# Optimization experiments

Measured on AMD Instinct MI355X. Metric: run time of the kernel, lower is better.

Reference implementation:

```python
import jax, jax.numpy as jnp
import numpy as np


def setup_inputs() -> dict:
    key = jax.random.key(0)
    k1, k2 = jax.random.split(key)
    num_tokens, top_k, num_experts = 1048576, 8, 64
    top_scores = jax.random.uniform(k1, (num_tokens, top_k), dtype=jnp.float32)
    selected_experts_indices = jax.random.randint(
        k2, (num_tokens, top_k), 0, num_experts, dtype=jnp.int64
    ) if jax.config.jax_enable_x64 else jax.random.randint(
        k2, (num_tokens, top_k), 0, num_experts, dtype=jnp.int32
    )
    return {
        "top_scores": top_scores,
        "selected_experts_indices": selected_experts_indices,
        "num_experts": num_experts,
    }


def reference(top_scores, selected_experts_indices, num_experts):
    flat_idx = selected_experts_indices.reshape(-1)  # [num_tokens*top_k]
    # histogram of tokens per expert (torch.histc returns float)
    num_tokens_per_expert = jnp.bincount(flat_idx, length=num_experts).astype(jnp.float32)
    # stable argsort by expert id -> permutation grouping tokens by expert
    token_indices_experts_sorted = jnp.argsort(flat_idx, stable=True)
    # gather routing scores into expert-sorted order
    top_scores_experts_sorted = top_scores.reshape(-1)[token_indices_experts_sorted]
    return (
        top_scores_experts_sorted,
        token_indices_experts_sorted,
        num_tokens_per_expert,
    )
```

## Files before the change

kernel.cpp:

```cpp
#include <hip/hip_runtime.h>


#define TILE 4096
#define WAVES 8
#define WCH  512
#define RND  8
#define TPB  512

__device__ __forceinline__ unsigned long long match_mask(
    unsigned key,
    unsigned long long b0, unsigned long long b1, unsigned long long b2,
    unsigned long long b3, unsigned long long b4, unsigned long long b5,
    unsigned long long am) {
  unsigned long long m = am;
  m &= (key & 1u)  ? b0 : ~b0;
  m &= (key & 2u)  ? b1 : ~b1;
  m &= (key & 4u)  ? b2 : ~b2;
  m &= (key & 8u)  ? b3 : ~b3;
  m &= (key & 16u) ? b4 : ~b4;
  m &= (key & 32u) ? b5 : ~b5;
  return m;
}

__global__ __launch_bounds__(256) void hist_kernel(
    const int* __restrict__ idx, unsigned* __restrict__ countsT,
    int N, int nb) {
  __shared__ unsigned h[4][64];
  const int wave = threadIdx.x >> 6;
  const int lane = threadIdx.x & 63;

  long long base = (long long)blockIdx.x * TILE;
  long long rem = (long long)N - base;
  unsigned cnt = 0;

  if (rem >= TILE) {
    const int4* v = (const int4*)(idx + base);
    unsigned es[16];
    #pragma unroll
    for (int k = 0; k < 4; ++k) {
      int4 x = v[threadIdx.x + k * 256];
      es[k * 4 + 0] = ((unsigned)x.x) & 63u;
      es[k * 4 + 1] = ((unsigned)x.y) & 63u;
      es[k * 4 + 2] = ((unsigned)x.z) & 63u;
      es[k * 4 + 3] = ((unsigned)x.w) & 63u;
    }
    #pragma unroll
    for (int r = 0; r < 16; ++r) {
      unsigned e = es[r];
      unsigned long long b0 = __ballot(e & 1u);
      unsigned long long b1 = __ballot(e & 2u);
      unsigned long long b2 = __ballot(e & 4u);
      unsigned long long b3 = __ballot(e & 8u);
      unsigned long long b4 = __ballot(e & 16u);
      unsigned long long b5 = __ballot(e & 32u);
      cnt += (unsigned)__popcll(
          match_mask((unsigned)lane, b0, b1, b2, b3, b4, b5, ~0ull));
    }
  } else {
    long long wstart = base + (long long)wave * 1024;
    for (int r = 0; r < 16; ++r) {
      long long i = wstart + (long long)r * 64 + lane;
      bool valid = i < (long long)N;
      unsigned long long am = __ballot(valid ? 1 : 0);
      unsigned e = valid ? (((unsigned)idx[i]) & 63u) : 0u;
      unsigned long long b0 = __ballot(e & 1u);
      unsigned long long b1 = __ballot(e & 2u);
      unsigned long long b2 = __ballot(e & 4u);
      unsigned long long b3 = __ballot(e & 8u);
      unsigned long long b4 = __ballot(e & 16u);
      unsigned long long b5 = __ballot(e & 32u);
      cnt += (unsigned)__popcll(
          match_mask((unsigned)lane, b0, b1, b2, b3, b4, b5, am));
    }
  }

  h[wave][lane] = cnt;
  __syncthreads();
  if (threadIdx.x < 64) {
    countsT[(size_t)blockIdx.x * 64 + threadIdx.x] =
        h[0][threadIdx.x] + h[1][threadIdx.x] + h[2][threadIdx.x] + h[3][threadIdx.x];
  }
}

__global__ __launch_bounds__(256) void scan_kernel(
    unsigned* __restrict__ countsT, unsigned* __restrict__ totals,
    float* __restrict__ out_counts, int nb) {
  const int e = blockIdx.x;
  const int t = threadIdx.x;
  const int wave = t >> 6;
  const int lane = t & 63;

  __shared__ unsigned buf[2048];
  __shared__ unsigned wsum[4];

  unsigned carry = 0;
  for (int c = 0; c < nb; c += 2048) {
    int m = nb - c; if (m > 2048) m = 2048;
    for (int j = t; j < 2048; j += 256)
      buf[j] = (j < m) ? countsT[(size_t)(c + j) * 64 + e] : 0u;
    __syncthreads();
    unsigned v[8]; unsigned s = 0;
    #pragma unroll
    for (int k = 0; k < 8; ++k) { v[k] = buf[t * 8 + k]; s += v[k]; }
    unsigned inc = s;
    #pragma unroll
    for (int d = 1; d < 64; d <<= 1) {
      unsigned nv = __shfl_up(inc, d, 64);
      if (lane >= d) inc += nv;
    }
    if (lane == 63) wsum[wave] = inc;
    __syncthreads();
    unsigned woff = 0;
    for (int w = 0; w < wave; ++w) woff += wsum[w];
    unsigned btot = wsum[0] + wsum[1] + wsum[2] + wsum[3];
    unsigned run = carry + woff + (inc - s);
    #pragma unroll
    for (int k = 0; k < 8; ++k) { buf[t * 8 + k] = run; run += v[k]; }
    __syncthreads();
    for (int j = t; j < 2048; j += 256)
      if (j < m) countsT[(size_t)(c + j) * 64 + e] = buf[j];
    carry += btot;
    __syncthreads();
  }
  if (t == 0) {
    totals[e] = carry;
    out_counts[e] = (float)carry;
  }
}

__global__ __launch_bounds__(TPB, 8) void scatter_kernel(
    const int* __restrict__ idx, const float* __restrict__ scores,
    const unsigned* __restrict__ baseT, const unsigned* __restrict__ totals,
    float* __restrict__ out_scores, float* __restrict__ out_idx,
    int N, int nb) {
  __shared__ __align__(16) uint2 sdat[TILE];
  __shared__ __align__(16) unsigned char tmpb[WAVES][64][RND];
  __shared__ unsigned shc[WAVES][64];
  __shared__ unsigned gdest[64];

  const int t = threadIdx.x;
  const int wave = t >> 6;
  const int lane = t & 63;
  const unsigned long long lt = (1ull << lane) - 1ull;

  const long long base = (long long)blockIdx.x * TILE;
  const long long start = base + (long long)wave * WCH;
  const bool fullt = (base + TILE) <= (long long)N;

  const unsigned tot = totals[lane];
  const unsigned gb0 = baseT[(size_t)blockIdx.x * 64 + lane];

  unsigned e_pk[2] = {0, 0};
  unsigned r_pk[2] = {0, 0};
  float    sreg[RND];
  unsigned c_pk[2];
  unsigned wtotal = 0;

  unsigned* idxs = (unsigned*)sdat;

  if (fullt) {
    {
      const int4* gi = (const int4*)(idx + base);
      int4 a0 = gi[t];
      int4 a1 = gi[t + 512];
      #pragma unroll
      for (int r = 0; r < RND; ++r) sreg[r] = scores[start + r * 64 + lane];
      ((int4*)idxs)[t] = a0;
      ((int4*)idxs)[t + 512] = a1;
    }
    *(uint2*)(&tmpb[wave][lane][0]) = make_uint2(0u, 0u);
    __syncthreads();

    #pragma unroll
    for (int r = 0; r < RND; ++r) {
      unsigned e = idxs[wave * WCH + r * 64 + lane] & 63u;
      unsigned long long b0 = __ballot(e & 1u);
      unsigned long long b1 = __ballot(e & 2u);
      unsigned long long b2 = __ballot(e & 4u);
      unsigned long long b3 = __ballot(e & 8u);
      unsigned long long b4 = __ballot(e & 16u);
      unsigned long long b5 = __ballot(e & 32u);
      unsigned long long ms = match_mask(e, b0, b1, b2, b3, b4, b5, ~0ull);
      unsigned rank = (unsigned)__popcll(ms & lt);
      unsigned rcnt = (unsigned)__popcll(ms);
      if (rank == 0) tmpb[wave][e][r] = (unsigned char)rcnt;
      const int q = r >> 2, sh = (r & 3) * 8;
      e_pk[q] |= e << sh;
      r_pk[q] |= rank << sh;
    }
    uint2 cw = *(const uint2*)(&tmpb[wave][lane][0]);
    c_pk[0] = cw.x; c_pk[1] = cw.y;
  } else {
    for (int j = t; j < TILE; j += TPB) sdat[j].y = 0xFFFFFFFFu;
    *(uint2*)(&tmpb[wave][lane][0]) = make_uint2(0u, 0u);
    __syncthreads();
    for (int r = 0; r < RND; ++r) {
      long long i = start + (long long)r * 64 + lane;
      bool valid = i < (long long)N;
      unsigned long long am = __ballot(valid ? 1 : 0);
      unsigned e = valid ? (((unsigned)idx[i]) & 63u) : 0u;
      sreg[r] = valid ? scores[i] : 0.0f;
      unsigned long long b0 = __ballot(e & 1u);
      unsigned long long b1 = __ballot(e & 2u);
      unsigned long long b2 = __ballot(e & 4u);
      unsigned long long b3 = __ballot(e & 8u);
      unsigned long long b4 = __ballot(e & 16u);
      unsigned long long b5 = __ballot(e & 32u);
      unsigned long long ms = match_mask(e, b0, b1, b2, b3, b4, b5, am);
      unsigned rank = (unsigned)__popcll(ms & lt);
      unsigned rcnt = (unsigned)__popcll(ms);
      if (valid && rank == 0) tmpb[wave][e][r] = (unsigned char)rcnt;
      const int q = r >> 2, sh = (r & 3) * 8;
      e_pk[q] |= e << sh;
      r_pk[q] |= rank << sh;
    }
    uint2 cw = *(const uint2*)(&tmpb[wave][lane][0]);
    c_pk[0] = cw.x; c_pk[1] = cw.y;
  }

  {
    unsigned acc = 0;
    #pragma unroll
    for (int q = 0; q < 2; ++q)
      acc += (c_pk[q] & 0x00FF00FFu) + ((c_pk[q] >> 8) & 0x00FF00FFu);
    wtotal = (acc & 0xFFFFu) + (acc >> 16);
  }

  shc[wave][lane] = wtotal;
  __syncthreads();

  unsigned cw_[WAVES];
  unsigned bt = 0;
  #pragma unroll
  for (int w = 0; w < WAVES; ++w) { cw_[w] = shc[w][lane]; bt += cw_[w]; }
  unsigned wpre = 0;
  #pragma unroll
  for (int w = 0; w < WAVES; ++w) if (w < wave) wpre += cw_[w];

  unsigned s = bt;
  #pragma unroll
  for (int d = 1; d < 64; d <<= 1) {
    unsigned nv = __shfl_up(s, d, 64);
    if (lane >= d) s += nv;
  }
  unsigned bstart = s - bt;
  unsigned wbase = bstart + wpre;

  unsigned cur[RND];
  {
    unsigned acc = wbase;
    #pragma unroll
    for (int r = 0; r < RND; ++r) {
      cur[r] = acc;
      acc += (c_pk[r >> 2] >> ((r & 3) * 8)) & 0xffu;
    }
  }

  if (wave == 0) {
    unsigned s2 = tot;
    #pragma unroll
    for (int d = 1; d < 64; d <<= 1) {
      unsigned nv = __shfl_up(s2, d, 64);
      if (lane >= d) s2 += nv;
    }
    unsigned estart = s2 - tot;
    gdest[lane] = estart + gb0 - bstart;
  }

  if (fullt) {
    #pragma unroll
    for (int r = 0; r < RND; ++r) {
      unsigned i32 = (unsigned)start + r * 64 + lane;
      const int q = r >> 2, sh = (r & 3) * 8;
      unsigned e    = (e_pk[q] >> sh) & 0xffu;
      unsigned rank = (r_pk[q] >> sh) & 0xffu;
      unsigned pos = (unsigned)__shfl((int)cur[r], (int)e, 64) + rank;
      sdat[pos] = make_uint2(__float_as_uint(sreg[r]), (i32 << 6) | e);
    }
  } else {
    for (int r = 0; r < RND; ++r) {
      long long i = start + (long long)r * 64 + lane;
      bool valid = i < (long long)N;
      const int q = r >> 2, sh = (r & 3) * 8;
      unsigned e    = (e_pk[q] >> sh) & 0xffu;
      unsigned rank = (r_pk[q] >> sh) & 0xffu;
      unsigned pos = (unsigned)__shfl((int)cur[r], (int)e, 64) + rank;
      if (valid) {
        sdat[pos] = make_uint2(__float_as_uint(sreg[r]), (((unsigned)i) << 6) | e);
      }
    }
  }
  __syncthreads();

  if (fullt) {
    #pragma unroll
    for (int k = 0; k < TILE / TPB; ++k) {
      int j = t + k * TPB;
      uint2 v = sdat[j];
      unsigned e = v.y & 63u;
      unsigned d = gdest[e] + (unsigned)j;
      out_scores[d] = __uint_as_float(v.x);
      out_idx[d] = (float)(v.y >> 6);
    }
  } else {
    for (int j = t; j < TILE; j += TPB) {
      uint2 v = sdat[j];
      if (v.y == 0xFFFFFFFFu) continue;
      unsigned e = v.y & 63u;
      unsigned d = gdest[e] + (unsigned)j;
      out_scores[d] = __uint_as_float(v.x);
      out_idx[d] = (float)(v.y >> 6);
    }
  }
}

extern "C" void kernel_launch(void* const* d_in, const int* in_sizes, int n_in,
                              void* d_out, int out_size, void* d_ws, size_t ws_size,
                              hipStream_t stream) {
  const float* scores = (const float*)d_in[0];
  const int* idx = (const int*)d_in[1];
  int N = in_sizes[0];

  float* out_scores = (float*)d_out;
  float* out_idx = out_scores + N;
  float* out_counts = out_idx + N;

  int nb = (N + TILE - 1) / TILE;
  unsigned* countsT = (unsigned*)d_ws;
  unsigned* totals = countsT + (size_t)nb * 64;

  hist_kernel<<<nb, 256, 0, stream>>>(idx, countsT, N, nb);
  scan_kernel<<<64, 256, 0, stream>>>(countsT, totals, out_counts, nb);
  scatter_kernel<<<nb, TPB, 0, stream>>>(idx, scores, countsT, totals,
                                         out_scores, out_idx, N, nb);
}
```

Before: 139.8 us.

## Make scatter kernel persistent and prefetch next tile during output writes

The scatter kernel becomes a grid-stride persistent kernel capped at 1024 blocks. The expert-offset scan over totals is computed once per block instead of once per tile. The next tile's indices and scores are loaded into registers while the current tile's scattered outputs are being written. This aims to hide global load latency and cut per-block setup overhead, but it adds an extra barrier per tile and may leave fewer blocks in flight to hide memory latency.

```diff
diff --git a/kernel.cpp b/kernel.cpp
--- a/kernel.cpp
+++ b/kernel.cpp
@@ -143,174 +143,187 @@
   const int lane = t & 63;
   const unsigned long long lt = (1ull << lane) - 1ull;
 
-  const long long base = (long long)blockIdx.x * TILE;
-  const long long start = base + (long long)wave * WCH;
-  const bool fullt = (base + TILE) <= (long long)N;
-
-  const unsigned tot = totals[lane];
-  const unsigned gb0 = baseT[(size_t)blockIdx.x * 64 + lane];
-
-  unsigned e_pk[2] = {0, 0};
-  unsigned r_pk[2] = {0, 0};
-  float    sreg[RND];
-  unsigned c_pk[2];
-  unsigned wtotal = 0;
-
   unsigned* idxs = (unsigned*)sdat;
 
-  if (fullt) {
-    {
-      const int4* gi = (const int4*)(idx + base);
-      int4 a0 = gi[t];
-      int4 a1 = gi[t + 512];
-      #pragma unroll
-      for (int r = 0; r < RND; ++r) sreg[r] = scores[start + r * 64 + lane];
-      ((int4*)idxs)[t] = a0;
-      ((int4*)idxs)[t + 512] = a1;
-    }
-    *(uint2*)(&tmpb[wave][lane][0]) = make_uint2(0u, 0u);
-    __syncthreads();
-
-    #pragma unroll
-    for (int r = 0; r < RND; ++r) {
-      unsigned e = idxs[wave * WCH + r * 64 + lane] & 63u;
-      unsigned long long b0 = __ballot(e & 1u);
-      unsigned long long b1 = __ballot(e & 2u);
-      unsigned long long b2 = __ballot(e & 4u);
-      unsigned long long b3 = __ballot(e & 8u);
-      unsigned long long b4 = __ballot(e & 16u);
-      unsigned long long b5 = __ballot(e & 32u);
-      unsigned long long ms = match_mask(e, b0, b1, b2, b3, b4, b5, ~0ull);
-      unsigned rank = (unsigned)__popcll(ms & lt);
-      unsigned rcnt = (unsigned)__popcll(ms);
-      if (rank == 0) tmpb[wave][e][r] = (unsigned char)rcnt;
-      const int q = r >> 2, sh = (r & 3) * 8;
-      e_pk[q] |= e << sh;
-      r_pk[q] |= rank << sh;
-    }
-    uint2 cw = *(const uint2*)(&tmpb[wave][lane][0]);
-    c_pk[0] = cw.x; c_pk[1] = cw.y;
-  } else {
-    for (int j = t; j < TILE; j += TPB) sdat[j].y = 0xFFFFFFFFu;
-    *(uint2*)(&tmpb[wave][lane][0]) = make_uint2(0u, 0u);
-    __syncthreads();
-    for (int r = 0; r < RND; ++r) {
-      long long i = start + (long long)r * 64 + lane;
-      bool valid = i < (long long)N;
-      unsigned long long am = __ballot(valid ? 1 : 0);
-      unsigned e = valid ? (((unsigned)idx[i]) & 63u) : 0u;
-      sreg[r] = valid ? scores[i] : 0.0f;
-      unsigned long long b0 = __ballot(e & 1u);
-      unsigned long long b1 = __ballot(e & 2u);
-      unsigned long long b2 = __ballot(e & 4u);
-      unsigned long long b3 = __ballot(e & 8u);
-      unsigned long long b4 = __ballot(e & 16u);
-      unsigned long long b5 = __ballot(e & 32u);
-      unsigned long long ms = match_mask(e, b0, b1, b2, b3, b4, b5, am);
-      unsigned rank = (unsigned)__popcll(ms & lt);
-      unsigned rcnt = (unsigned)__popcll(ms);
-      if (valid && rank == 0) tmpb[wave][e][r] = (unsigned char)rcnt;
-      const int q = r >> 2, sh = (r & 3) * 8;
-      e_pk[q] |= e << sh;
-      r_pk[q] |= rank << sh;
-    }
-    uint2 cw = *(const uint2*)(&tmpb[wave][lane][0]);
-    c_pk[0] = cw.x; c_pk[1] = cw.y;
-  }
-
+  unsigned estart;
   {
-    unsigned acc = 0;
-    #pragma unroll
-    for (int q = 0; q < 2; ++q)
-      acc += (c_pk[q] & 0x00FF00FFu) + ((c_pk[q] >> 8) & 0x00FF00FFu);
-    wtotal = (acc & 0xFFFFu) + (acc >> 16);
-  }
-
-  shc[wave][lane] = wtotal;
-  __syncthreads();
-
-  unsigned cw_[WAVES];
-  unsigned bt = 0;
-  #pragma unroll
-  for (int w = 0; w < WAVES; ++w) { cw_[w] = shc[w][lane]; bt += cw_[w]; }
-  unsigned wpre = 0;
-  #pragma unroll
-  for (int w = 0; w < WAVES; ++w) if (w < wave) wpre += cw_[w];
-
-  unsigned s = bt;
-  #pragma unroll
-  for (int d = 1; d < 64; d <<= 1) {
-    unsigned nv = __shfl_up(s, d, 64);
-    if (lane >= d) s += nv;
-  }
-  unsigned bstart = s - bt;
-  unsigned wbase = bstart + wpre;
-
-  unsigned cur[RND];
-  {
-    unsigned acc = wbase;
-    #pragma unroll
-    for (int r = 0; r < RND; ++r) {
-      cur[r] = acc;
-      acc += (c_pk[r >> 2] >> ((r & 3) * 8)) & 0xffu;
-    }
-  }
-
-  if (wave == 0) {
+    unsigned tot = totals[lane];
     unsigned s2 = tot;
     #pragma unroll
     for (int d = 1; d < 64; d <<= 1) {
       unsigned nv = __shfl_up(s2, d, 64);
       if (lane >= d) s2 += nv;
     }
-    unsigned estart = s2 - tot;
-    gdest[lane] = estart + gb0 - bstart;
-  }
-
-  if (fullt) {
-    #pragma unroll
-    for (int r = 0; r < RND; ++r) {
-      unsigned i32 = (unsigned)start + r * 64 + lane;
-      const int q = r >> 2, sh = (r & 3) * 8;
-      unsigned e    = (e_pk[q] >> sh) & 0xffu;
-      unsigned rank = (r_pk[q] >> sh) & 0xffu;
-      unsigned pos = (unsigned)__shfl((int)cur[r], (int)e, 64) + rank;
-      sdat[pos] = make_uint2(__float_as_uint(sreg[r]), (i32 << 6) | e);
-    }
-  } else {
-    for (int r = 0; r < RND; ++r) {
-      long long i = start + (long long)r * 64 + lane;
-      bool valid = i < (long long)N;
-      const int q = r >> 2, sh = (r & 3) * 8;
-      unsigned e    = (e_pk[q] >> sh) & 0xffu;
-      unsigned rank = (r_pk[q] >> sh) & 0xffu;
-      unsigned pos = (unsigned)__shfl((int)cur[r], (int)e, 64) + rank;
-      if (valid) {
-        sdat[pos] = make_uint2(__float_as_uint(sreg[r]), (((unsigned)i) << 6) | e);
-      }
-    }
-  }
-  __syncthreads();
-
-  if (fullt) {
-    #pragma unroll
-    for (int k = 0; k < TILE / TPB; ++k) {
-      int j = t + k * TPB;
-      uint2 v = sdat[j];
-      unsigned e = v.y & 63u;
-      unsigned d = gdest[e] + (unsigned)j;
-      out_scores[d] = __uint_as_float(v.x);
-      out_idx[d] = (float)(v.y >> 6);
-    }
-  } else {
-    for (int j = t; j < TILE; j += TPB) {
-      uint2 v = sdat[j];
-      if (v.y == 0xFFFFFFFFu) continue;
-      unsigned e = v.y & 63u;
-      unsigned d = gdest[e] + (unsigned)j;
-      out_scores[d] = __uint_as_float(v.x);
-      out_idx[d] = (float)(v.y >> 6);
-    }
+    estart = s2 - tot;
+  }
+
+  int tile = blockIdx.x;
+  int4 a0, a1;
+  float sreg[RND];
+
+  if (tile < nb && ((long long)(tile + 1) * TILE) <= (long long)N) {
+    const long long base = (long long)tile * TILE;
+    const int4* gi = (const int4*)(idx + base);
+    a0 = gi[t];
+    a1 = gi[t + 512];
+    const long long start = base + (long long)wave * WCH;
+    #pragma unroll
+    for (int r = 0; r < RND; ++r) sreg[r] = scores[start + r * 64 + lane];
+  }
+
+  while (tile < nb) {
+    const long long base = (long long)tile * TILE;
+    const long long start = base + (long long)wave * WCH;
+    const bool fullt = (base + TILE) <= (long long)N;
+    const unsigned gb0 = baseT[(size_t)tile * 64 + lane];
+    const int next = tile + (int)gridDim.x;
+
+    unsigned e_pk[2] = {0, 0};
+    unsigned r_pk[2] = {0, 0};
+    unsigned c_pk[2];
+
+    if (fullt) {
+      ((int4*)idxs)[t] = a0;
+      ((int4*)idxs)[t + 512] = a1;
+      *(uint2*)(&tmpb[wave][lane][0]) = make_uint2(0u, 0u);
+      __syncthreads();
+
+      #pragma unroll
+      for (int r = 0; r < RND; ++r) {
+        unsigned e = idxs[wave * WCH + r * 64 + lane] & 63u;
+        unsigned long long b0 = __ballot(e & 1u);
+        unsigned long long b1 = __ballot(e & 2u);
+        unsigned long long b2 = __ballot(e & 4u);
+        unsigned long long b3 = __ballot(e & 8u);
+        unsigned long long b4 = __ballot(e & 16u);
+        unsigned long long b5 = __ballot(e & 32u);
+        unsigned long long ms = match_mask(e, b0, b1, b2, b3, b4, b5, ~0ull);
+        unsigned rank = (unsigned)__popcll(ms & lt);
+        unsigned rcnt = (unsigned)__popcll(ms);
+        if (rank == 0) tmpb[wave][e][r] = (unsigned char)rcnt;
+        const int q = r >> 2, sh = (r & 3) * 8;
+        e_pk[q] |= e << sh;
+        r_pk[q] |= rank << sh;
+      }
+      uint2 cw = *(const uint2*)(&tmpb[wave][lane][0]);
+      c_pk[0] = cw.x; c_pk[1] = cw.y;
+    } else {
+      for (int j = t; j < TILE; j += TPB) sdat[j].y = 0xFFFFFFFFu;
+      *(uint2*)(&tmpb[wave][lane][0]) = make_uint2(0u, 0u);
+      __syncthreads();
+      for (int r = 0; r < RND; ++r) {
+        long long i = start + (long long)r * 64 + lane;
+        bool valid = i < (long long)N;
+        unsigned long long am = __ballot(valid ? 1 : 0);
+        unsigned e = valid ? (((unsigned)idx[i]) & 63u) : 0u;
+        sreg[r] = valid ? scores[i] : 0.0f;
+        unsigned long long b0 = __ballot(e & 1u);
+        unsigned long long b1 = __ballot(e & 2u);
+        unsigned long long b2 = __ballot(e & 4u);
+        unsigned long long b3 = __ballot(e & 8u);
+        unsigned long long b4 = __ballot(e & 16u);
+        unsigned long long b5 = __ballot(e & 32u);
+        unsigned long long ms = match_mask(e, b0, b1, b2, b3, b4, b5, am);
+        unsigned rank = (unsigned)__popcll(ms & lt);
+        unsigned rcnt = (unsigned)__popcll(ms);
+        if (valid && rank == 0) tmpb[wave][e][r] = (unsigned char)rcnt;
+        const int q = r >> 2, sh = (r & 3) * 8;
+        e_pk[q] |= e << sh;
+        r_pk[q] |= rank << sh;
+      }
+      uint2 cw = *(const uint2*)(&tmpb[wave][lane][0]);
+      c_pk[0] = cw.x; c_pk[1] = cw.y;
+    }
+
+    unsigned wtotal;
+    {
+      unsigned acc = (c_pk[0] & 0x00FF00FFu) + ((c_pk[0] >> 8) & 0x00FF00FFu)
+                   + (c_pk[1] & 0x00FF00FFu) + ((c_pk[1] >> 8) & 0x00FF00FFu);
+      wtotal = (acc & 0xFFFFu) + (acc >> 16);
+    }
+
+    shc[wave][lane] = wtotal;
+    __syncthreads();
+
+    unsigned bt = 0, wpre = 0;
+    #pragma unroll
+    for (int w = 0; w < WAVES; ++w) {
+      unsigned c = shc[w][lane];
+      bt += c;
+      if (w < wave) wpre += c;
+    }
+
+    unsigned s = bt;
+    #pragma unroll
+    for (int d = 1; d < 64; d <<= 1) {
+      unsigned nv = __shfl_up(s, d, 64);
+      if (lane >= d) s += nv;
+    }
+    unsigned bstart = s - bt;
+    unsigned wbase = bstart + wpre;
+
+    if (wave == 0) gdest[lane] = estart + gb0 - bstart;
+
+    unsigned cur_r = wbase;
+    if (fullt) {
+      #pragma unroll
+      for (int r = 0; r < RND; ++r) {
+        unsigned i32 = (unsigned)start + r * 64 + lane;
+        const int q = r >> 2, sh = (r & 3) * 8;
+        unsigned e    = (e_pk[q] >> sh) & 0xffu;
+        unsigned rank = (r_pk[q] >> sh) & 0xffu;
+        unsigned pos = (unsigned)__shfl((int)cur_r, (int)e, 64) + rank;
+        sdat[pos] = make_uint2(__float_as_uint(sreg[r]), (i32 << 6) | e);
+        cur_r += (c_pk[q] >> sh) & 0xffu;
+      }
+    } else {
+      for (int r = 0; r < RND; ++r) {
+        long long i = start + (long long)r * 64 + lane;
+        bool valid = i < (long long)N;
+        const int q = r >> 2, sh = (r & 3) * 8;
+        unsigned e    = (e_pk[q] >> sh) & 0xffu;
+        unsigned rank = (r_pk[q] >> sh) & 0xffu;
+        unsigned pos = (unsigned)__shfl((int)cur_r, (int)e, 64) + rank;
+        if (valid) {
+          sdat[pos] = make_uint2(__float_as_uint(sreg[r]), (((unsigned)i) << 6) | e);
+        }
+        cur_r += (c_pk[q] >> sh) & 0xffu;
+      }
+    }
+    __syncthreads();
+
+    if (next < nb && ((long long)(next + 1) * TILE) <= (long long)N) {
+      const long long nbase = (long long)next * TILE;
+      const int4* gi = (const int4*)(idx + nbase);
+      a0 = gi[t];
+      a1 = gi[t + 512];
+      const long long nstart = nbase + (long long)wave * WCH;
+      #pragma unroll
+      for (int r = 0; r < RND; ++r) sreg[r] = scores[nstart + r * 64 + lane];
+    }
+
+    if (fullt) {
+      #pragma unroll
+      for (int k = 0; k < TILE / TPB; ++k) {
+        int j = t + k * TPB;
+        uint2 v = sdat[j];
+        unsigned e = v.y & 63u;
+        unsigned d = gdest[e] + (unsigned)j;
+        out_scores[d] = __uint_as_float(v.x);
+        out_idx[d] = (float)(v.y >> 6);
+      }
+    } else {
+      for (int j = t; j < TILE; j += TPB) {
+        uint2 v = sdat[j];
+        if (v.y == 0xFFFFFFFFu) continue;
+        unsigned e = v.y & 63u;
+        unsigned d = gdest[e] + (unsigned)j;
+        out_scores[d] = __uint_as_float(v.x);
+        out_idx[d] = (float)(v.y >> 6);
+      }
+    }
+    __syncthreads();
+    tile = next;
   }
 }
 
@@ -329,8 +342,10 @@
   unsigned* countsT = (unsigned*)d_ws;
   unsigned* totals = countsT + (size_t)nb * 64;
 
+  int sgrid = nb < 1024 ? nb : 1024;
+
   hist_kernel<<<nb, 256, 0, stream>>>(idx, countsT, N, nb);
   scan_kernel<<<64, 256, 0, stream>>>(countsT, totals, out_counts, nb);
-  scatter_kernel<<<nb, TPB, 0, stream>>>(idx, scores, countsT, totals,
-                                         out_scores, out_idx, N, nb);
-}
+  scatter_kernel<<<sgrid, TPB, 0, stream>>>(idx, scores, countsT, totals,
+                                            out_scores, out_idx, N, nb);
+}
```

Result: slower. 167.8 us (+20.0%).
